# Optimization experiments

Measured on AMD Instinct MI355X. Metric: run time of the kernel, lower is better.

## Reference

```python
import jax, jax.numpy as jnp
import numpy as np

N_NODES = 100000
N_EDGES = 1600000
D_IN = 64
D_OUT = 64


def setup_inputs() -> dict:
    key = jax.random.key(0)
    k1, k2, k3, k4, k5, k6 = jax.random.split(key, 6)
    feat = jax.random.normal(k1, (N_NODES, D_IN), dtype=jnp.float32)
    src = jax.random.randint(k2, (N_EDGES,), 0, N_NODES, dtype=jnp.int64)
    dst = jax.random.randint(k3, (N_EDGES,), 0, N_NODES, dtype=jnp.int64)
    edge_weight = jax.random.uniform(k4, (N_EDGES,), dtype=jnp.float32)
    # Xavier-uniform with relu gain, as in reset_parameters
    gain = float(np.sqrt(2.0))
    bound = gain * float(np.sqrt(6.0 / (D_IN + D_OUT)))
    W_neigh = jax.random.uniform(k5, (D_OUT, D_IN), dtype=jnp.float32, minval=-bound, maxval=bound)
    W_self = jax.random.uniform(k6, (D_OUT, D_IN), dtype=jnp.float32, minval=-bound, maxval=bound)
    bias = jnp.zeros((D_OUT,), dtype=jnp.float32)
    return {"feat": feat, "src": src, "dst": dst, "edge_weight": edge_weight,
            "W_neigh": W_neigh, "W_self": W_self, "bias": bias}


def reference(feat, src, dst, edge_weight, W_neigh, W_self, bias):
    n = feat.shape[0]
    # feat_drop with p=0.0 is identity; in_feats == out_feats so lin_before_mp is False
    # message: u_mul_e -> gather src features, scale by edge weight  [E, D_IN]
    m = feat[src] * edge_weight[:, None]
    # mean reduce over incoming edges (zero for isolated dst nodes, matching DGL)
    s = jax.ops.segment_sum(m, dst, num_segments=n)
    deg = jax.ops.segment_sum(jnp.ones_like(edge_weight), dst, num_segments=n)
    neigh = s / jnp.maximum(deg, 1.0)[:, None]
    h_neigh = neigh @ W_neigh.T
    h_self = feat @ W_self.T
    return h_self + h_neigh + bias
```

## Files before the change

kernel.cpp:

```cpp
#include <hip/hip_runtime.h>
#include <hip/hip_fp16.h>

constexpr int N_NODES = 100000;
constexpr int N_EDGES = 1600000;
constexpr int D = 64;

constexpr int BSH    = 6;
constexpr int BN     = 1 << BSH;
constexpr int NBUCK  = (N_NODES + BN - 1) / BN;
constexpr int NN2    = NBUCK * BN;
constexpr int NCNTB  = 800;
constexpr int EPB2   = N_EDGES / NCNTB;
constexpr int NCVT   = (N_NODES * D / 4) / 256;
constexpr int NBINS  = (NN2 + 1023) >> 10;
constexpr int CHUNK  = 2048;
constexpr int NPA    = (N_EDGES + CHUNK - 1) / CHUNK;

constexpr size_t OFF_NSTART   = 400384;
constexpr size_t OFF_BINCNT   = 800768;
constexpr size_t OFF_BINSTART = 801280;
constexpr size_t OFF_BINCUR   = 801792;
constexpr size_t OFF_W16      = 1602048;
constexpr size_t OFF_FEAT16   = 1634816;
constexpr size_t OFF_ENT2     = OFF_FEAT16 + (size_t)N_NODES * D * 2;
constexpr size_t OFF_ENTA     = OFF_ENT2 + (size_t)N_EDGES * 8;
constexpr size_t WS_NEEDED    = OFF_ENTA + (size_t)N_EDGES * 8;

typedef short  bf16x8 __attribute__((ext_vector_type(8)));
typedef float  f32x4  __attribute__((ext_vector_type(4)));

__device__ __forceinline__ unsigned short f2bf(float f) {
    unsigned u = __float_as_uint(f);
    u += 0x7fffu + ((u >> 16) & 1u);
    return (unsigned short)(u >> 16);
}

__device__ __forceinline__ float h2f_lo(unsigned u) {
    return __half2float(__ushort_as_half((unsigned short)(u & 0xFFFFu)));
}
__device__ __forceinline__ float h2f_hi(unsigned u) {
    return __half2float(__ushort_as_half((unsigned short)(u >> 16)));
}

__device__ __forceinline__ void split8(float4 p0, float4 p1, bf16x8& hi, bf16x8& lo) {
    float f[8] = {p0.x, p0.y, p0.z, p0.w, p1.x, p1.y, p1.z, p1.w};
#pragma unroll
    for (int i = 0; i < 8; ++i) {
        const unsigned short h = f2bf(f[i]);
        const float hf = __uint_as_float((unsigned)h << 16);
        hi[i] = (short)h;
        lo[i] = (short)f2bf(f[i] - hf);
    }
}

__global__ __launch_bounds__(256) void k_zero(int* __restrict__ bincnt) {
    int i = blockIdx.x * 256 + threadIdx.x;
    if (i < NBINS) bincnt[i] = 0;
}

__global__ __launch_bounds__(256) void k_pre(const float4* __restrict__ feat4,
                                             unsigned short* __restrict__ feat16,
                                             const float* __restrict__ Wn,
                                             const float* __restrict__ Ws,
                                             unsigned short* __restrict__ W16,
                                             const int* __restrict__ dst,
                                             int* __restrict__ bincnt) {
    __shared__ int l[NBINS];
    const int b   = blockIdx.x;
    const int tid = threadIdx.x;
    if (b < NCVT) {
        const int i = b * 256 + tid;
        float4 v = feat4[i];
        ushort4 o;
        o.x = __half_as_ushort(__float2half_rn(v.x));
        o.y = __half_as_ushort(__float2half_rn(v.y));
        o.z = __half_as_ushort(__float2half_rn(v.z));
        o.w = __half_as_ushort(__float2half_rn(v.w));
        *(ushort4*)&feat16[(size_t)i * 4] = o;
    } else if (b < NCVT + NCNTB) {
        for (int i = tid; i < NBINS; i += 256) l[i] = 0;
        __syncthreads();
        const int base = (b - NCVT) * EPB2;
        for (int k = tid; k < EPB2; k += 256)
            atomicAdd(&l[dst[base + k] >> 10], 1);
        __syncthreads();
        for (int i = tid; i < NBINS; i += 256)
            if (l[i]) atomicAdd(&bincnt[i], l[i]);
    } else {
        for (int e = tid; e < D * 128; e += 256) {
            const int j = e >> 7, k = e & 127;
            const float w = (k < D) ? Ws[j * D + k] : Wn[j * D + (k - D)];
            const unsigned short h = f2bf(w);
            const float hf = __uint_as_float((unsigned)h << 16);
            W16[e] = h;
            W16[D * 128 + e] = f2bf(w - hf);
        }
    }
}

__global__ __launch_bounds__(128) void k_scan_bins(const int* __restrict__ bincnt,
                                                   int* __restrict__ binstart,
                                                   int* __restrict__ bincur) {
    __shared__ int s[128];
    const int t = threadIdx.x;
    const int v = (t < NBINS) ? bincnt[t] : 0;
    s[t] = v;
    __syncthreads();
    for (int off = 1; off < 128; off <<= 1) {
        int u = (t >= off) ? s[t - off] : 0;
        __syncthreads();
        s[t] += u;
        __syncthreads();
    }
    if (t < NBINS) { binstart[t] = s[t] - v; bincur[t] = s[t] - v; }
    if (t == 0) binstart[NBINS] = N_EDGES;
}

__global__ __launch_bounds__(256) void k_place_a(const int* __restrict__ src,
                                                 const int* __restrict__ dst,
                                                 const float* __restrict__ ew,
                                                 int* __restrict__ bincur,
                                                 uint2* __restrict__ entriesA) {
    __shared__ __align__(16) uint2 stage[CHUNK];
    __shared__ unsigned char sbin[CHUNK];
    __shared__ int hist[NBINS], lstart[NBINS], lcur[NBINS], gbase[NBINS];
    __shared__ int s[256];
    const int tid = threadIdx.x;
    const int e0  = blockIdx.x * CHUNK;
    const int cnt = min(CHUNK, N_EDGES - e0);

    for (int i = tid; i < NBINS; i += 256) hist[i] = 0;
    __syncthreads();
    for (int k = tid; k < cnt; k += 256)
        atomicAdd(&hist[dst[e0 + k] >> 10], 1);
    __syncthreads();
    {
        const int v = (tid < NBINS) ? hist[tid] : 0;
        s[tid] = v;
        __syncthreads();
        for (int off = 1; off < 256; off <<= 1) {
            int u = (tid >= off) ? s[tid - off] : 0;
            __syncthreads();
            s[tid] += u;
            __syncthreads();
        }
        if (tid < NBINS) {
            const int ex = s[tid] - v;
            lstart[tid] = ex;
            lcur[tid]   = ex;
            gbase[tid]  = v ? atomicAdd(&bincur[tid], v) : 0;
        }
    }
    __syncthreads();
    for (int k = tid; k < cnt; k += 256) {
        const int d = dst[e0 + k];
        const int b = d >> 10;
        const int p = atomicAdd(&lcur[b], 1);
        stage[p] = make_uint2((unsigned)src[e0 + k] | ((unsigned)(d & 1023) << 17),
                              __float_as_uint(ew[e0 + k]));
        sbin[p]  = (unsigned char)b;
    }
    __syncthreads();
    for (int j = tid; j < cnt; j += 256) {
        const int b = sbin[j];
        entriesA[gbase[b] + (j - lstart[b])] = stage[j];
    }
}

__global__ __launch_bounds__(1024) void k_sortbin(const int* __restrict__ binstart,
                                                  const uint2* __restrict__ entriesA,
                                                  int* __restrict__ nstart,
                                                  uint2* __restrict__ entries2) {
    __shared__ int h[1024];
    __shared__ int s[1024];
    __shared__ int cur[1024];
    const int tid = threadIdx.x;
    const int b   = blockIdx.x;
    const int s0  = binstart[b];
    const int cnt = binstart[b + 1] - s0;

    h[tid] = 0;
    __syncthreads();
    for (int k = tid; k < cnt; k += 1024)
        atomicAdd(&h[entriesA[s0 + k].x >> 17], 1);
    __syncthreads();
    const int v = h[tid];
    s[tid] = v;
    __syncthreads();
    for (int off = 1; off < 1024; off <<= 1) {
        int u = (tid >= off) ? s[tid - off] : 0;
        __syncthreads();
        s[tid] += u;
        __syncthreads();
    }
    const int pos = s0 + s[tid] - v;
    cur[tid] = pos;
    const int n = (b << 10) + tid;
    if (n < NN2) nstart[n] = pos;
    if (b == NBINS - 1 && tid == 0) nstart[NN2] = N_EDGES;
    __syncthreads();
    for (int k = tid; k < cnt; k += 1024) {
        const uint2 a = entriesA[s0 + k];
        const int p = atomicAdd(&cur[a.x >> 17], 1);
        entries2[p] = make_uint2(a.x & 0x1FFFFu, a.y);
    }
}

__global__ __launch_bounds__(256, 8) void k_bucket(
    const uint2* __restrict__ feat16u2,
    const float* __restrict__ feat32,
    const int* __restrict__ nstart,
    const uint2* __restrict__ entries2,
    const unsigned short* __restrict__ W16,
    const float* __restrict__ bias,
    float* __restrict__ out) {
    __shared__ __align__(16) float aggrow[BN * 68];
    __shared__ int hh[BN], st[BN];
    const int tid = threadIdx.x;
    const int b   = blockIdx.x;

    if (tid < BN) {
        const int s = nstart[b * BN + tid];
        const int e = nstart[b * BN + tid + 1];
        st[tid] = s;
        hh[tid] = e - s;
    }
    __syncthreads();

    const int wave = tid >> 6, lane = tid & 63;
    const int group = lane >> 4, gl = lane & 15;
    for (int t = 0; t < 16; ++t) {
        const int dl  = wave * 16 + t;
        const int ss  = st[dl];
        const int deg = hh[dl];
        const int se  = ss + deg;
        float4 acc = make_float4(0.f, 0.f, 0.f, 0.f);
        int e = ss + group;
        for (; e + 12 < se; e += 16) {
            const uint2 en0 = entries2[e];
            const uint2 en1 = entries2[e + 4];
            const uint2 en2 = entries2[e + 8];
            const uint2 en3 = entries2[e + 12];
            const uint2 p0  = feat16u2[(size_t)en0.x * 16 + gl];
            const uint2 p1  = feat16u2[(size_t)en1.x * 16 + gl];
            const uint2 p2  = feat16u2[(size_t)en2.x * 16 + gl];
            const uint2 p3  = feat16u2[(size_t)en3.x * 16 + gl];
            const float w0  = __uint_as_float(en0.y);
            const float w1  = __uint_as_float(en1.y);
            const float w2  = __uint_as_float(en2.y);
            const float w3  = __uint_as_float(en3.y);
            acc.x = fmaf(h2f_lo(p0.x), w0, acc.x);
            acc.y = fmaf(h2f_hi(p0.x), w0, acc.y);
            acc.z = fmaf(h2f_lo(p0.y), w0, acc.z);
            acc.w = fmaf(h2f_hi(p0.y), w0, acc.w);
            acc.x = fmaf(h2f_lo(p1.x), w1, acc.x);
            acc.y = fmaf(h2f_hi(p1.x), w1, acc.y);
            acc.z = fmaf(h2f_lo(p1.y), w1, acc.z);
            acc.w = fmaf(h2f_hi(p1.y), w1, acc.w);
            acc.x = fmaf(h2f_lo(p2.x), w2, acc.x);
            acc.y = fmaf(h2f_hi(p2.x), w2, acc.y);
            acc.z = fmaf(h2f_lo(p2.y), w2, acc.z);
            acc.w = fmaf(h2f_hi(p2.y), w2, acc.w);
            acc.x = fmaf(h2f_lo(p3.x), w3, acc.x);
            acc.y = fmaf(h2f_hi(p3.x), w3, acc.y);
            acc.z = fmaf(h2f_lo(p3.y), w3, acc.z);
            acc.w = fmaf(h2f_hi(p3.y), w3, acc.w);
        }
        for (; e < se; e += 4) {
            const uint2 en = entries2[e];
            const float w  = __uint_as_float(en.y);
            const uint2 p  = feat16u2[(size_t)en.x * 16 + gl];
            acc.x = fmaf(h2f_lo(p.x), w, acc.x);
            acc.y = fmaf(h2f_hi(p.x), w, acc.y);
            acc.z = fmaf(h2f_lo(p.y), w, acc.z);
            acc.w = fmaf(h2f_hi(p.y), w, acc.w);
        }
#pragma unroll
        for (int m = 16; m <= 32; m <<= 1) {
            acc.x += __shfl_xor(acc.x, m);
            acc.y += __shfl_xor(acc.y, m);
            acc.z += __shfl_xor(acc.z, m);
            acc.w += __shfl_xor(acc.w, m);
        }
        if (group == 0) {
            const float inv = 1.0f / fmaxf((float)deg, 1.0f);
            float4 o = make_float4(acc.x * inv, acc.y * inv, acc.z * inv, acc.w * inv);
            *(float4*)&aggrow[dl * 68 + gl * 4] = o;
        }
    }
    __syncthreads();

    const int quad = lane >> 4, r = lane & 15;
    const int node0 = b * BN + wave * 16;
    int arow = node0 + r;
    if (arow > N_NODES - 1) arow = N_NODES - 1;

    bf16x8 ahi[4], alo[4];
    {
        const float* fp = &feat32[(size_t)arow * 64 + quad * 8];
        split8(*(const float4*)fp,        *(const float4*)(fp + 4),  ahi[0], alo[0]);
        split8(*(const float4*)(fp + 32), *(const float4*)(fp + 36), ahi[1], alo[1]);
        const float* ap = &aggrow[(wave * 16 + r) * 68 + quad * 8];
        split8(*(const float4*)ap,        *(const float4*)(ap + 4),  ahi[2], alo[2]);
        split8(*(const float4*)(ap + 32), *(const float4*)(ap + 36), ahi[3], alo[3]);
    }

    const unsigned short* W16lo = W16 + D * 128;
    f32x4 acc4[4] = {};
#pragma unroll
    for (int nt = 0; nt < 4; ++nt) {
#pragma unroll
        for (int kc = 0; kc < 4; ++kc) {
            const size_t wo = (size_t)(nt * 16 + r) * 128 + kc * 32 + quad * 8;
            const bf16x8 bhi = *(const bf16x8*)&W16[wo];
            const bf16x8 blo = *(const bf16x8*)&W16lo[wo];
            acc4[nt] = __builtin_amdgcn_mfma_f32_16x16x32_bf16(ahi[kc], bhi, acc4[nt], 0, 0, 0);
            acc4[nt] = __builtin_amdgcn_mfma_f32_16x16x32_bf16(alo[kc], bhi, acc4[nt], 0, 0, 0);
            acc4[nt] = __builtin_amdgcn_mfma_f32_16x16x32_bf16(ahi[kc], blo, acc4[nt], 0, 0, 0);
        }
    }

#pragma unroll
    for (int nt = 0; nt < 4; ++nt) {
        const float bv = bias[nt * 16 + r];
#pragma unroll
        for (int reg = 0; reg < 4; ++reg) {
            const int m = node0 + quad * 4 + reg;
            if (m < N_NODES) out[(size_t)m * 64 + nt * 16 + r] = acc4[nt][reg] + bv;
        }
    }
}

__global__ __launch_bounds__(256) void fb_zero(float4* __restrict__ out4,
                                               float* __restrict__ deg) {
    const int stride = gridDim.x * blockDim.x;
    int i = blockIdx.x * blockDim.x + threadIdx.x;
    const int total4 = (N_NODES * D) / 4;
    for (int idx = i; idx < total4; idx += stride)
        out4[idx] = make_float4(0.f, 0.f, 0.f, 0.f);
    for (int idx = i; idx < N_NODES; idx += stride)
        deg[idx] = 0.f;
}

__global__ __launch_bounds__(256) void fb_scatter(
    const float* __restrict__ feat, const int* __restrict__ src,
    const int* __restrict__ dst, const float* __restrict__ ew,
    float* __restrict__ out, float* __restrict__ deg) {
    const int gid  = blockIdx.x * blockDim.x + threadIdx.x;
    const int e    = gid >> 6;
    const int lane = gid & 63;
    if (e >= N_EDGES) return;
    atomicAdd(&out[(size_t)dst[e] * D + lane], feat[(size_t)src[e] * D + lane] * ew[e]);
    if (lane == 0) atomicAdd(&deg[dst[e]], 1.0f);
}

__global__ __launch_bounds__(256) void fb_finalize(
    const float* __restrict__ feat, const float* __restrict__ Wn,
    const float* __restrict__ Ws, const float* __restrict__ bias,
    const float* __restrict__ deg, float* __restrict__ out) {
    __shared__ float lWn[D * 65];
    __shared__ float lWs[D * 65];
    for (int idx = threadIdx.x; idx < D * D; idx += 256) {
        const int r = idx >> 6, c = idx & 63;
        lWn[r * 65 + c] = Wn[idx];
        lWs[r * 65 + c] = Ws[idx];
    }
    __syncthreads();
    const int wave = threadIdx.x >> 6;
    const int lane = threadIdx.x & 63;
    const int n = blockIdx.x * 4 + wave;
    if (n >= N_NODES) return;
    const float f  = feat[(size_t)n * D + lane];
    const float sv = out[(size_t)n * D + lane];
    const float inv = 1.0f / fmaxf(deg[n], 1.0f);
    float acc_s = 0.f, acc_n = 0.f;
#pragma unroll
    for (int k = 0; k < D; ++k) {
        acc_s += __shfl(f, k)  * lWs[lane * 65 + k];
        acc_n += __shfl(sv, k) * lWn[lane * 65 + k];
    }
    out[(size_t)n * D + lane] = acc_s + acc_n * inv + bias[lane];
}

extern "C" void kernel_launch(void* const* d_in, const int* in_sizes, int n_in,
                              void* d_out, int out_size, void* d_ws, size_t ws_size,
                              hipStream_t stream) {
    const float* feat = (const float*)d_in[0];
    const int*   src  = (const int*)  d_in[1];
    const int*   dst  = (const int*)  d_in[2];
    const float* ew   = (const float*)d_in[3];
    const float* Wn   = (const float*)d_in[4];
    const float* Ws   = (const float*)d_in[5];
    const float* bias = (const float*)d_in[6];
    float* out = (float*)d_out;
    char* ws = (char*)d_ws;

    if (ws_size >= WS_NEEDED) {
        int* nstart   = (int*)(ws + OFF_NSTART);
        int* bincnt   = (int*)(ws + OFF_BINCNT);
        int* binstart = (int*)(ws + OFF_BINSTART);
        int* bincur   = (int*)(ws + OFF_BINCUR);
        unsigned short* W16    = (unsigned short*)(ws + OFF_W16);
        unsigned short* feat16 = (unsigned short*)(ws + OFF_FEAT16);
        uint2* entries2 = (uint2*)(ws + OFF_ENT2);
        uint2* entriesA = (uint2*)(ws + OFF_ENTA);

        k_zero     <<<1, 256, 0, stream>>>(bincnt);
        k_pre      <<<NCVT + NCNTB + 1, 256, 0, stream>>>((const float4*)feat, feat16,
                                                          Wn, Ws, W16, dst, bincnt);
        k_scan_bins<<<1, 128, 0, stream>>>(bincnt, binstart, bincur);
        k_place_a  <<<NPA, 256, 0, stream>>>(src, dst, ew, bincur, entriesA);
        k_sortbin  <<<NBINS, 1024, 0, stream>>>(binstart, entriesA, nstart, entries2);
        k_bucket   <<<NBUCK, 256, 0, stream>>>((const uint2*)feat16, feat, nstart,
                                               entries2, W16, bias, out);
    } else {
        float* deg = (float*)d_ws;
        fb_zero<<<2048, 256, 0, stream>>>((float4*)out, deg);
        fb_scatter<<<(N_EDGES * 64) / 256, 256, 0, stream>>>(feat, src, dst, ew, out, deg);
        fb_finalize<<<(N_NODES + 3) / 4, 256, 0, stream>>>(feat, Wn, Ws, bias, deg, out);
    }
}
```

Baseline: 246.4 us.

## Halve bucket and sort-bin sizes, split MFMA output columns across waves

Shrinks the node bucket per block from 64 to 32 nodes and the counting-sort bin from 1024 to 512 nodes. This doubles the number of blocks in the aggregation and sort kernels, for more parallelism and better load balance. The edge loop unroll drops from 4 to 2 edges in flight. Each wave now computes half the output columns for 16 rows rather than all columns, so the W fragment loads are duplicated across waves and there is less memory-level parallelism per thread.

```diff
diff --git a/kernel.cpp b/kernel.cpp
--- a/kernel.cpp
+++ b/kernel.cpp
@@ -5,21 +5,23 @@
 constexpr int N_EDGES = 1600000;
 constexpr int D = 64;
 
-constexpr int BSH    = 6;
+constexpr int BSH    = 5;
 constexpr int BN     = 1 << BSH;
-constexpr int NBUCK  = (N_NODES + BN - 1) / BN;
-constexpr int NN2    = NBUCK * BN;
+constexpr int NBUCK  = N_NODES / BN;
+constexpr int NN2    = N_NODES;
 constexpr int NCNTB  = 800;
 constexpr int EPB2   = N_EDGES / NCNTB;
 constexpr int NCVT   = (N_NODES * D / 4) / 256;
-constexpr int NBINS  = (NN2 + 1023) >> 10;
+constexpr int BINSH  = 9;
+constexpr int BINSZ  = 1 << BINSH;
+constexpr int NBINS  = (NN2 + BINSZ - 1) >> BINSH;
 constexpr int CHUNK  = 2048;
 constexpr int NPA    = (N_EDGES + CHUNK - 1) / CHUNK;
 
 constexpr size_t OFF_NSTART   = 400384;
 constexpr size_t OFF_BINCNT   = 800768;
 constexpr size_t OFF_BINSTART = 801280;
-constexpr size_t OFF_BINCUR   = 801792;
+constexpr size_t OFF_BINCUR   = 802304;
 constexpr size_t OFF_W16      = 1602048;
 constexpr size_t OFF_FEAT16   = 1634816;
 constexpr size_t OFF_ENT2     = OFF_FEAT16 + (size_t)N_NODES * D * 2;
@@ -82,7 +84,7 @@
         __syncthreads();
         const int base = (b - NCVT) * EPB2;
         for (int k = tid; k < EPB2; k += 256)
-            atomicAdd(&l[dst[base + k] >> 10], 1);
+            atomicAdd(&l[dst[base + k] >> BINSH], 1);
         __syncthreads();
         for (int i = tid; i < NBINS; i += 256)
             if (l[i]) atomicAdd(&bincnt[i], l[i]);
@@ -98,15 +100,15 @@
     }
 }
 
-__global__ __launch_bounds__(128) void k_scan_bins(const int* __restrict__ bincnt,
+__global__ __launch_bounds__(256) void k_scan_bins(const int* __restrict__ bincnt,
                                                    int* __restrict__ binstart,
                                                    int* __restrict__ bincur) {
-    __shared__ int s[128];
+    __shared__ int s[256];
     const int t = threadIdx.x;
     const int v = (t < NBINS) ? bincnt[t] : 0;
     s[t] = v;
     __syncthreads();
-    for (int off = 1; off < 128; off <<= 1) {
+    for (int off = 1; off < 256; off <<= 1) {
         int u = (t >= off) ? s[t - off] : 0;
         __syncthreads();
         s[t] += u;
@@ -132,7 +134,7 @@
     for (int i = tid; i < NBINS; i += 256) hist[i] = 0;
     __syncthreads();
     for (int k = tid; k < cnt; k += 256)
-        atomicAdd(&hist[dst[e0 + k] >> 10], 1);
+        atomicAdd(&hist[dst[e0 + k] >> BINSH], 1);
     __syncthreads();
     {
         const int v = (tid < NBINS) ? hist[tid] : 0;
@@ -154,9 +156,9 @@
     __syncthreads();
     for (int k = tid; k < cnt; k += 256) {
         const int d = dst[e0 + k];
-        const int b = d >> 10;
+        const int b = d >> BINSH;
         const int p = atomicAdd(&lcur[b], 1);
-        stage[p] = make_uint2((unsigned)src[e0 + k] | ((unsigned)(d & 1023) << 17),
+        stage[p] = make_uint2((unsigned)src[e0 + k] | ((unsigned)(d & (BINSZ - 1)) << 17),
                               __float_as_uint(ew[e0 + k]));
         sbin[p]  = (unsigned char)b;
     }
@@ -171,32 +173,35 @@
                                                   const uint2* __restrict__ entriesA,
                                                   int* __restrict__ nstart,
                                                   uint2* __restrict__ entries2) {
-    __shared__ int h[1024];
-    __shared__ int s[1024];
-    __shared__ int cur[1024];
+    __shared__ int h[BINSZ];
+    __shared__ int sc[BINSZ];
+    __shared__ int cur[BINSZ];
     const int tid = threadIdx.x;
     const int b   = blockIdx.x;
     const int s0  = binstart[b];
     const int cnt = binstart[b + 1] - s0;
 
-    h[tid] = 0;
+    if (tid < BINSZ) h[tid] = 0;
     __syncthreads();
     for (int k = tid; k < cnt; k += 1024)
         atomicAdd(&h[entriesA[s0 + k].x >> 17], 1);
     __syncthreads();
-    const int v = h[tid];
-    s[tid] = v;
-    __syncthreads();
-    for (int off = 1; off < 1024; off <<= 1) {
-        int u = (tid >= off) ? s[tid - off] : 0;
-        __syncthreads();
-        s[tid] += u;
-        __syncthreads();
-    }
-    const int pos = s0 + s[tid] - v;
-    cur[tid] = pos;
-    const int n = (b << 10) + tid;
-    if (n < NN2) nstart[n] = pos;
+    const int v = (tid < BINSZ) ? h[tid] : 0;
+    if (tid < BINSZ) sc[tid] = v;
+    __syncthreads();
+    for (int off = 1; off < BINSZ; off <<= 1) {
+        int u = 0;
+        if (tid < BINSZ && tid >= off) u = sc[tid - off];
+        __syncthreads();
+        if (tid < BINSZ) sc[tid] += u;
+        __syncthreads();
+    }
+    if (tid < BINSZ) {
+        const int pos = s0 + sc[tid] - v;
+        cur[tid] = pos;
+        const int n = (b << BINSH) + tid;
+        if (n < NN2) nstart[n] = pos;
+    }
     if (b == NBINS - 1 && tid == 0) nstart[NN2] = N_EDGES;
     __syncthreads();
     for (int k = tid; k < cnt; k += 1024) {
@@ -229,26 +234,20 @@
 
     const int wave = tid >> 6, lane = tid & 63;
     const int group = lane >> 4, gl = lane & 15;
-    for (int t = 0; t < 16; ++t) {
-        const int dl  = wave * 16 + t;
+    for (int t = 0; t < 8; ++t) {
+        const int dl  = wave * 8 + t;
         const int ss  = st[dl];
         const int deg = hh[dl];
         const int se  = ss + deg;
         float4 acc = make_float4(0.f, 0.f, 0.f, 0.f);
         int e = ss + group;
-        for (; e + 12 < se; e += 16) {
+        for (; e + 4 < se; e += 8) {
             const uint2 en0 = entries2[e];
             const uint2 en1 = entries2[e + 4];
-            const uint2 en2 = entries2[e + 8];
-            const uint2 en3 = entries2[e + 12];
             const uint2 p0  = feat16u2[(size_t)en0.x * 16 + gl];
             const uint2 p1  = feat16u2[(size_t)en1.x * 16 + gl];
-            const uint2 p2  = feat16u2[(size_t)en2.x * 16 + gl];
-            const uint2 p3  = feat16u2[(size_t)en3.x * 16 + gl];
             const float w0  = __uint_as_float(en0.y);
             const float w1  = __uint_as_float(en1.y);
-            const float w2  = __uint_as_float(en2.y);
-            const float w3  = __uint_as_float(en3.y);
             acc.x = fmaf(h2f_lo(p0.x), w0, acc.x);
             acc.y = fmaf(h2f_hi(p0.x), w0, acc.y);
             acc.z = fmaf(h2f_lo(p0.y), w0, acc.z);
@@ -257,16 +256,8 @@
             acc.y = fmaf(h2f_hi(p1.x), w1, acc.y);
             acc.z = fmaf(h2f_lo(p1.y), w1, acc.z);
             acc.w = fmaf(h2f_hi(p1.y), w1, acc.w);
-            acc.x = fmaf(h2f_lo(p2.x), w2, acc.x);
-            acc.y = fmaf(h2f_hi(p2.x), w2, acc.y);
-            acc.z = fmaf(h2f_lo(p2.y), w2, acc.z);
-            acc.w = fmaf(h2f_hi(p2.y), w2, acc.w);
-            acc.x = fmaf(h2f_lo(p3.x), w3, acc.x);
-            acc.y = fmaf(h2f_hi(p3.x), w3, acc.y);
-            acc.z = fmaf(h2f_lo(p3.y), w3, acc.z);
-            acc.w = fmaf(h2f_hi(p3.y), w3, acc.w);
-        }
-        for (; e < se; e += 4) {
+        }
+        if (e < se) {
             const uint2 en = entries2[e];
             const float w  = __uint_as_float(en.y);
             const uint2 p  = feat16u2[(size_t)en.x * 16 + gl];
@@ -291,7 +282,8 @@
     __syncthreads();
 
     const int quad = lane >> 4, r = lane & 15;
-    const int node0 = b * BN + wave * 16;
+    const int rowh = wave & 1, colh = wave >> 1;
+    const int node0 = b * BN + rowh * 16;
     int arow = node0 + r;
     if (arow > N_NODES - 1) arow = N_NODES - 1;
 
@@ -300,33 +292,35 @@
         const float* fp = &feat32[(size_t)arow * 64 + quad * 8];
         split8(*(const float4*)fp,        *(const float4*)(fp + 4),  ahi[0], alo[0]);
         split8(*(const float4*)(fp + 32), *(const float4*)(fp + 36), ahi[1], alo[1]);
-        const float* ap = &aggrow[(wave * 16 + r) * 68 + quad * 8];
+        const float* ap = &aggrow[(rowh * 16 + r) * 68 + quad * 8];
         split8(*(const float4*)ap,        *(const float4*)(ap + 4),  ahi[2], alo[2]);
         split8(*(const float4*)(ap + 32), *(const float4*)(ap + 36), ahi[3], alo[3]);
     }
 
     const unsigned short* W16lo = W16 + D * 128;
-    f32x4 acc4[4] = {};
-#pragma unroll
-    for (int nt = 0; nt < 4; ++nt) {
+    f32x4 acc4[2] = {};
+#pragma unroll
+    for (int nti = 0; nti < 2; ++nti) {
+        const int nt = colh * 2 + nti;
 #pragma unroll
         for (int kc = 0; kc < 4; ++kc) {
             const size_t wo = (size_t)(nt * 16 + r) * 128 + kc * 32 + quad * 8;
             const bf16x8 bhi = *(const bf16x8*)&W16[wo];
             const bf16x8 blo = *(const bf16x8*)&W16lo[wo];
-            acc4[nt] = __builtin_amdgcn_mfma_f32_16x16x32_bf16(ahi[kc], bhi, acc4[nt], 0, 0, 0);
-            acc4[nt] = __builtin_amdgcn_mfma_f32_16x16x32_bf16(alo[kc], bhi, acc4[nt], 0, 0, 0);
-            acc4[nt] = __builtin_amdgcn_mfma_f32_16x16x32_bf16(ahi[kc], blo, acc4[nt], 0, 0, 0);
-        }
-    }
-
-#pragma unroll
-    for (int nt = 0; nt < 4; ++nt) {
+            acc4[nti] = __builtin_amdgcn_mfma_f32_16x16x32_bf16(ahi[kc], bhi, acc4[nti], 0, 0, 0);
+            acc4[nti] = __builtin_amdgcn_mfma_f32_16x16x32_bf16(alo[kc], bhi, acc4[nti], 0, 0, 0);
+            acc4[nti] = __builtin_amdgcn_mfma_f32_16x16x32_bf16(ahi[kc], blo, acc4[nti], 0, 0, 0);
+        }
+    }
+
+#pragma unroll
+    for (int nti = 0; nti < 2; ++nti) {
+        const int nt = colh * 2 + nti;
         const float bv = bias[nt * 16 + r];
 #pragma unroll
         for (int reg = 0; reg < 4; ++reg) {
             const int m = node0 + quad * 4 + reg;
-            if (m < N_NODES) out[(size_t)m * 64 + nt * 16 + r] = acc4[nt][reg] + bv;
+            if (m < N_NODES) out[(size_t)m * 64 + nt * 16 + r] = acc4[nti][reg] + bv;
         }
     }
 }
@@ -408,7 +402,7 @@
         k_zero     <<<1, 256, 0, stream>>>(bincnt);
         k_pre      <<<NCVT + NCNTB + 1, 256, 0, stream>>>((const float4*)feat, feat16,
                                                           Wn, Ws, W16, dst, bincnt);
-        k_scan_bins<<<1, 128, 0, stream>>>(bincnt, binstart, bincur);
+        k_scan_bins<<<1, 256, 0, stream>>>(bincnt, binstart, bincur);
         k_place_a  <<<NPA, 256, 0, stream>>>(src, dst, ew, bincur, entriesA);
         k_sortbin  <<<NBINS, 1024, 0, stream>>>(binstart, entriesA, nstart, entries2);
         k_bucket   <<<NBUCK, 256, 0, stream>>>((const uint2*)feat16, feat, nstart,
```

New measurement: 240.4 us. -2.4%, faster.
